# Kernel optimization log

Measured on AMD Instinct MI355X. Metric: run time of the kernel, lower is better.

## Reference

```python
import jax, jax.numpy as jnp
import numpy as np

N = 50000   # nodes
E = 800000  # edges (avg degree 16)
F_IN = 128
H = 128
L = 4
LN_EPS = 1e-5


def setup_inputs() -> dict:
    key = jax.random.key(0)
    ks = jax.random.split(key, 4)
    x = jax.random.normal(ks[0], (N, F_IN), dtype=jnp.float32)
    edge_index = jax.random.randint(ks[1], (2, E), 0, N)
    conv_w = jax.random.normal(ks[2], (L, F_IN, H), dtype=jnp.float32) * 0.05
    conv_b = jnp.zeros((L, H), dtype=jnp.float32)
    ln_g = jnp.ones((L, H), dtype=jnp.float32)
    ln_b = jnp.zeros((L, H), dtype=jnp.float32)
    head_w = jax.random.normal(ks[3], (H, 1), dtype=jnp.float32) * 0.05
    head_b = jnp.zeros((1,), dtype=jnp.float32)
    return {"x": x, "edge_index": edge_index, "conv_w": conv_w, "conv_b": conv_b,
            "ln_g": ln_g, "ln_b": ln_b, "head_w": head_w, "head_b": head_b}


def _layer_norm(h, g, b):
    mu = jnp.mean(h, axis=-1, keepdims=True)
    var = jnp.mean(jnp.square(h - mu), axis=-1, keepdims=True)
    return (h - mu) * jax.lax.rsqrt(var + LN_EPS) * g + b


def _gcn_conv(h, W, b, src, dst, inv_sqrt_deg, inv_deg):
    # PyG GCNConv: self-loops + symmetric normalization D^-1/2 (A+I) D^-1/2, then bias.
    hw = h @ W  # (N, H)
    norm = inv_sqrt_deg[src] * inv_sqrt_deg[dst]  # (E,)
    msg = hw[src] * norm[:, None]  # gather + edgewise scale
    agg = jax.ops.segment_sum(msg, dst, num_segments=N)  # scatter-add
    agg = agg + hw * inv_deg[:, None]  # self-loop term (norm = 1/deg)
    return agg + b


def reference(x, edge_index, conv_w, conv_b, ln_g, ln_b, head_w, head_b):
    src, dst = edge_index[0], edge_index[1]
    # degree on target nodes, including self-loop
    deg = jax.ops.segment_sum(jnp.ones((E,), x.dtype), dst, num_segments=N) + 1.0
    inv_sqrt_deg = jax.lax.rsqrt(deg)
    inv_deg = 1.0 / deg
    h = x
    for i in range(L):
        h = _gcn_conv(h, conv_w[i], conv_b[i], src, dst, inv_sqrt_deg, inv_deg)
        h = _layer_norm(h, ln_g[i], ln_b[i])
        if i != L - 1:
            h = jax.nn.gelu(h, approximate=False)
            # dropout is identity in eval mode
    scores = (h @ head_w + head_b).squeeze(-1)  # (N,)
    return scores, h
```

## Files before the change

### kernel.cpp

```cpp
#include <hip/hip_runtime.h>
#include <math.h>

#define N_NODES 50000
#define N_EDGES 800000
#define HDIM 128
#define NLAYERS 4
#define LN_EPS 1e-5f
#define EQUARTER (N_EDGES / 4)
#define SEG 64
#define FILLB ((EQUARTER + 255) / 256)
#define GEMMB ((N_NODES + 63) / 64)

typedef __attribute__((ext_vector_type(8))) short short8;
typedef __attribute__((ext_vector_type(4))) float floatx4;

__device__ __forceinline__ ushort f2bf(float x) {
    unsigned b = __float_as_uint(x);
    unsigned r = b + 0x7fffu + ((b >> 16) & 1u);
    return (ushort)(r >> 16);
}
__device__ __forceinline__ float2 bf2f2(unsigned u) {
    return make_float2(__uint_as_float(u << 16), __uint_as_float(u & 0xffff0000u));
}


__device__ __forceinline__ void fill_body(int bid, int tid, const int* __restrict__ src,
                                          const int* __restrict__ dst, int* __restrict__ cnt,
                                          ushort* __restrict__ csr16) {
    int t = bid * 256 + tid;
    if (t >= EQUARTER) return;
    int s0 = src[t],                d0 = dst[t];
    int s1 = src[t + EQUARTER],     d1 = dst[t + EQUARTER];
    int s2 = src[t + 2 * EQUARTER], d2 = dst[t + 2 * EQUARTER];
    int s3 = src[t + 3 * EQUARTER], d3 = dst[t + 3 * EQUARTER];
    int p0 = atomicAdd(&cnt[d0], 1);
    int p1 = atomicAdd(&cnt[d1], 1);
    int p2 = atomicAdd(&cnt[d2], 1);
    int p3 = atomicAdd(&cnt[d3], 1);
    if (p0 < SEG) csr16[d0 * SEG + p0] = (ushort)s0;
    if (p1 < SEG) csr16[d1 * SEG + p1] = (ushort)s1;
    if (p2 < SEG) csr16[d2 * SEG + p2] = (ushort)s2;
    if (p3 < SEG) csr16[d3 * SEG + p3] = (ushort)s3;
}

__global__ __launch_bounds__(256) void isd_kernel(const int* __restrict__ cnt,
                                                  float* __restrict__ isd,
                                                  float* __restrict__ ind) {
    int i = blockIdx.x * 256 + threadIdx.x;
    if (i < N_NODES) {
        float d = (float)cnt[i] + 1.0f;
        isd[i] = rsqrtf(d);
        ind[i] = 1.0f / d;
    }
}

__global__ __launch_bounds__(256) void bprep_kernel(const float* __restrict__ W,
                                                    ushort* __restrict__ bfrag) {
    int idx = blockIdx.x * 256 + threadIdx.x;
    if (idx >= NLAYERS * 4 * 8 * 64) return;
    int lane = idx & 63;
    int t = (idx >> 6) & 7;
    int s = (idx >> 9) & 3;
    int l = idx >> 11;
    int n = t * 16 + (lane & 15);
    int kb = s * 32 + (lane >> 4) * 8;
    const float* Wl = W + (size_t)l * HDIM * HDIM;
    union { uint4 q; ushort u[8]; } o;
#pragma unroll
    for (int j = 0; j < 8; ++j) o.u[j] = f2bf(Wl[(size_t)(kb + j) * HDIM + n]);
    *(uint4*)&bfrag[(size_t)idx * 8] = o.q;
}

template <bool A_FP32>
__device__ __forceinline__ void gemm_body(int bid, int tid, const void* __restrict__ Av,
                                          const ushort* __restrict__ bfrag,
                                          ushort* __restrict__ out) {
    int wave = tid >> 6, lane = tid & 63;
    int quad = lane >> 4, mrow = lane & 15;
    int rowBase = bid * 64 + wave * 16;
    int arow = rowBase + mrow;
    bool aok = arow < N_NODES;

    floatx4 acc[8];
#pragma unroll
    for (int t = 0; t < 8; ++t) acc[t] = (floatx4)0.f;

#pragma unroll
    for (int s = 0; s < 4; ++s) {
        union { short8 v; ushort u[8]; } af;
        if (A_FP32) {
            const float* A = (const float*)Av;
            if (aok) {
                const float* p = &A[(size_t)arow * HDIM + s * 32 + quad * 8];
#pragma unroll
                for (int j = 0; j < 8; ++j) af.u[j] = f2bf(p[j]);
            } else {
#pragma unroll
                for (int j = 0; j < 8; ++j) af.u[j] = 0;
            }
        } else {
            const ushort* A = (const ushort*)Av;
            if (aok) {
                af.v = *(const short8*)&A[(size_t)arow * HDIM + s * 32 + quad * 8];
            } else {
#pragma unroll
                for (int j = 0; j < 8; ++j) af.u[j] = 0;
            }
        }
#pragma unroll
        for (int t = 0; t < 8; ++t) {
            short8 bf = *(const short8*)&bfrag[(size_t)(((s * 8 + t) * 64) + lane) * 8];
            acc[t] = __builtin_amdgcn_mfma_f32_16x16x32_bf16(af.v, bf, acc[t], 0, 0, 0);
        }
    }
#pragma unroll
    for (int t = 0; t < 8; ++t) {
#pragma unroll
        for (int r = 0; r < 4; ++r) {
            int row = rowBase + quad * 4 + r;
            if (row < N_NODES) out[(size_t)row * HDIM + t * 16 + mrow] = f2bf(acc[t][r]);
        }
    }
}

__global__ __launch_bounds__(256) void fused0_kernel(
    const int* __restrict__ src, const int* __restrict__ dst, int* __restrict__ cnt,
    ushort* __restrict__ csr16, const float* __restrict__ x,
    const ushort* __restrict__ bfrag0, ushort* __restrict__ hw) {
    if (blockIdx.x < FILLB)
        fill_body(blockIdx.x, threadIdx.x, src, dst, cnt, csr16);
    else
        gemm_body<true>(blockIdx.x - FILLB, threadIdx.x, x, bfrag0, hw);
}

__global__ __launch_bounds__(256) void agg_ln_kernel(
    const uint2* __restrict__ hw2, const int* __restrict__ degcnt,
    const ushort* __restrict__ csr16, const float* __restrict__ isd,
    const float* __restrict__ ind, const float* __restrict__ conv_b,
    const float* __restrict__ ln_g, const float* __restrict__ ln_b,
    uint2* __restrict__ hout_bf, float* __restrict__ hout_f32,
    const float* __restrict__ head_w, const float* __restrict__ head_b,
    float* __restrict__ scores, int final_layer) {
    int wave = threadIdx.x >> 6;
    int lane = threadIdx.x & 63;
    int g = lane >> 5;
    int li = lane & 31;
    int n = blockIdx.x * 4 + wave;
    if (n >= N_NODES) return;
    int c = li * 4;

    float isd_n = isd[n], ind_n = ind[n];
    int rs = n * SEG;
    int deg = min(degcnt[n], SEG);

    float e0 = 0.f, e1 = 0.f, e2 = 0.f, e3 = 0.f;
    int sj = 0;
    float wj = 0.f;
    if (lane < deg) {
        sj = (int)csr16[rs + lane];
        wj = isd[sj];
    }
    for (int j = 0; j < deg; j += 8) {
#pragma unroll
        for (int t = 0; t < 4; ++t) {
            int idx = j + 2 * t + g;
            int s = __shfl(sj, idx);
            float w = __shfl(wj, idx);
            uint2 u = hw2[(size_t)s * 32 + li];
            float2 q0 = bf2f2(u.x), q1 = bf2f2(u.y);
            e0 = fmaf(q0.x, w, e0); e1 = fmaf(q0.y, w, e1);
            e2 = fmaf(q1.x, w, e2); e3 = fmaf(q1.y, w, e3);
        }
    }
    e0 += __shfl_xor(e0, 32); e1 += __shfl_xor(e1, 32);
    e2 += __shfl_xor(e2, 32); e3 += __shfl_xor(e3, 32);

    uint2 hv = hw2[(size_t)n * 32 + li];
    float2 h0 = bf2f2(hv.x), h1 = bf2f2(hv.y);
    float4 cb = *(const float4*)&conv_b[c];
    float a0 = fmaf(e0, isd_n, fmaf(h0.x, ind_n, cb.x));
    float a1 = fmaf(e1, isd_n, fmaf(h0.y, ind_n, cb.y));
    float a2 = fmaf(e2, isd_n, fmaf(h1.x, ind_n, cb.z));
    float a3 = fmaf(e3, isd_n, fmaf(h1.y, ind_n, cb.w));

    float sum = a0 + a1 + a2 + a3;
#pragma unroll
    for (int o = 1; o < 32; o <<= 1) sum += __shfl_xor(sum, o);
    float mu = sum * (1.0f / HDIM);
    float d0 = a0 - mu, d1 = a1 - mu, d2 = a2 - mu, d3 = a3 - mu;
    float vs = d0 * d0 + d1 * d1 + d2 * d2 + d3 * d3;
#pragma unroll
    for (int o = 1; o < 32; o <<= 1) vs += __shfl_xor(vs, o);
    float rstd = rsqrtf(vs * (1.0f / HDIM) + LN_EPS);
    float4 gv = *(const float4*)&ln_g[c];
    float4 bv = *(const float4*)&ln_b[c];
    float y0 = fmaf(d0 * rstd, gv.x, bv.x);
    float y1 = fmaf(d1 * rstd, gv.y, bv.y);
    float y2 = fmaf(d2 * rstd, gv.z, bv.z);
    float y3 = fmaf(d3 * rstd, gv.w, bv.w);

    if (!final_layer) {
#define GELU(v) ((v) = 0.5f * (v) * (1.0f + erff((v) * 0.70710678118654752f)))
        GELU(y0); GELU(y1); GELU(y2); GELU(y3);
#undef GELU
        if (g == 0) {
            uint2 ov;
            ov.x = (unsigned)f2bf(y0) | ((unsigned)f2bf(y1) << 16);
            ov.y = (unsigned)f2bf(y2) | ((unsigned)f2bf(y3) << 16);
            hout_bf[(size_t)n * 32 + li] = ov;
        }
    } else {
        if (g == 0)
            *(float4*)&hout_f32[(size_t)n * HDIM + c] = make_float4(y0, y1, y2, y3);
        float4 hwv = *(const float4*)&head_w[c];
        float p = y0 * hwv.x + y1 * hwv.y + y2 * hwv.z + y3 * hwv.w;
#pragma unroll
        for (int o = 1; o < 32; o <<= 1) p += __shfl_xor(p, o);
        if (lane == 0) scores[n] = p + head_b[0];
    }
}

__global__ __launch_bounds__(256) void layer_fused_kernel(
    const uint2* __restrict__ h2, const int* __restrict__ degcnt,
    const ushort* __restrict__ csr16, const float* __restrict__ isd,
    const float* __restrict__ ind, const ushort* __restrict__ bfrag,
    const float* __restrict__ conv_b, const float* __restrict__ ln_g,
    const float* __restrict__ ln_b, uint2* __restrict__ hout_bf,
    float* __restrict__ hout_f32, const float* __restrict__ head_w,
    const float* __restrict__ head_b, float* __restrict__ scores,
    int final_layer) {
    __shared__ float aggsf[64][132];
    int wave = threadIdx.x >> 6, lane = threadIdx.x & 63;
    int g = lane >> 5, li = lane & 31;

    for (int it = 0; it < 16; ++it) {
        int rblk = wave * 16 + it;
        int n = blockIdx.x * 64 + rblk;
        float a0 = 0.f, a1 = 0.f, a2 = 0.f, a3 = 0.f;
        if (n < N_NODES) {
            float isd_n = isd[n], ind_n = ind[n];
            int rs = n * SEG;
            int deg = min(degcnt[n], SEG);
            float e0 = 0.f, e1 = 0.f, e2 = 0.f, e3 = 0.f;
            int sj = 0;
            float wj = 0.f;
            if (lane < deg) {
                sj = (int)csr16[rs + lane];
                wj = isd[sj];
            }
            for (int j = 0; j < deg; j += 8) {
#pragma unroll
                for (int t = 0; t < 4; ++t) {
                    int idx = j + 2 * t + g;
                    int s = __shfl(sj, idx);
                    float w = __shfl(wj, idx);
                    uint2 u = h2[(size_t)s * 32 + li];
                    float2 q0 = bf2f2(u.x), q1 = bf2f2(u.y);
                    e0 = fmaf(q0.x, w, e0); e1 = fmaf(q0.y, w, e1);
                    e2 = fmaf(q1.x, w, e2); e3 = fmaf(q1.y, w, e3);
                }
            }
            e0 += __shfl_xor(e0, 32); e1 += __shfl_xor(e1, 32);
            e2 += __shfl_xor(e2, 32); e3 += __shfl_xor(e3, 32);
            uint2 hv = h2[(size_t)n * 32 + li];
            float2 h0 = bf2f2(hv.x), h1v = bf2f2(hv.y);
            a0 = fmaf(e0, isd_n, h0.x * ind_n);
            a1 = fmaf(e1, isd_n, h0.y * ind_n);
            a2 = fmaf(e2, isd_n, h1v.x * ind_n);
            a3 = fmaf(e3, isd_n, h1v.y * ind_n);
        }
        if (g == 0)
            *(float4*)&aggsf[rblk][li * 4] = make_float4(a0, a1, a2, a3);
    }

    int quad = lane >> 4, mrow = lane & 15;
    floatx4 acc[8];
#pragma unroll
    for (int t = 0; t < 8; ++t) acc[t] = (floatx4)0.f;
#pragma unroll
    for (int s = 0; s < 4; ++s) {
        const float* rowp = &aggsf[wave * 16 + mrow][s * 32 + quad * 8];
        float4 pa = *(const float4*)rowp;
        float4 pb = *(const float4*)(rowp + 4);
        float p[8] = {pa.x, pa.y, pa.z, pa.w, pb.x, pb.y, pb.z, pb.w};
        union { short8 v; ushort u[8]; } hi, lo;
#pragma unroll
        for (int j = 0; j < 8; ++j) {
            ushort h = f2bf(p[j]);
            hi.u[j] = h;
            float hf = __uint_as_float((unsigned)h << 16);
            lo.u[j] = f2bf(p[j] - hf);
        }
#pragma unroll
        for (int t = 0; t < 8; ++t) {
            short8 bf = *(const short8*)&bfrag[(size_t)(((s * 8 + t) * 64) + lane) * 8];
            acc[t] = __builtin_amdgcn_mfma_f32_16x16x32_bf16(lo.v, bf, acc[t], 0, 0, 0);
            acc[t] = __builtin_amdgcn_mfma_f32_16x16x32_bf16(hi.v, bf, acc[t], 0, 0, 0);
        }
    }

    {
        float cb[8];
#pragma unroll
        for (int t = 0; t < 8; ++t) cb[t] = conv_b[t * 16 + mrow];
#pragma unroll
        for (int t = 0; t < 8; ++t)
#pragma unroll
            for (int r = 0; r < 4; ++r)
                aggsf[wave * 16 + quad * 4 + r][t * 16 + mrow] = acc[t][r] + cb[t];
    }

    int c = li * 4;
    float4 gv = *(const float4*)&ln_g[c];
    float4 bv = *(const float4*)&ln_b[c];
    float4 hwv = *(const float4*)&head_w[c];
    for (int it = 0; it < 16; ++it) {
        int row = wave * 16 + it;
        int n = blockIdx.x * 64 + row;
        if (n >= N_NODES) continue;
        float4 v = *(const float4*)&aggsf[row][c];
        float a0 = v.x, a1 = v.y, a2 = v.z, a3 = v.w;

        float sum = a0 + a1 + a2 + a3;
#pragma unroll
        for (int o = 1; o < 32; o <<= 1) sum += __shfl_xor(sum, o);
        float mu = sum * (1.0f / HDIM);
        float d0 = a0 - mu, d1 = a1 - mu, d2 = a2 - mu, d3 = a3 - mu;
        float vs = d0 * d0 + d1 * d1 + d2 * d2 + d3 * d3;
#pragma unroll
        for (int o = 1; o < 32; o <<= 1) vs += __shfl_xor(vs, o);
        float rstd = rsqrtf(vs * (1.0f / HDIM) + LN_EPS);
        float y0 = fmaf(d0 * rstd, gv.x, bv.x);
        float y1 = fmaf(d1 * rstd, gv.y, bv.y);
        float y2 = fmaf(d2 * rstd, gv.z, bv.z);
        float y3 = fmaf(d3 * rstd, gv.w, bv.w);

        if (!final_layer) {
#define GELU(v) ((v) = 0.5f * (v) * (1.0f + erff((v) * 0.70710678118654752f)))
            GELU(y0); GELU(y1); GELU(y2); GELU(y3);
#undef GELU
            if (g == 0) {
                uint2 ov;
                ov.x = (unsigned)f2bf(y0) | ((unsigned)f2bf(y1) << 16);
                ov.y = (unsigned)f2bf(y2) | ((unsigned)f2bf(y3) << 16);
                hout_bf[(size_t)n * 32 + li] = ov;
            }
        } else {
            if (g == 0)
                *(float4*)&hout_f32[(size_t)n * HDIM + c] = make_float4(y0, y1, y2, y3);
            float p = y0 * hwv.x + y1 * hwv.y + y2 * hwv.z + y3 * hwv.w;
#pragma unroll
            for (int o = 1; o < 32; o <<= 1) p += __shfl_xor(p, o);
            if (lane == 0) scores[n] = p + head_b[0];
        }
    }
}


extern "C" void kernel_launch(void* const* d_in, const int* in_sizes, int n_in,
                              void* d_out, int out_size, void* d_ws, size_t ws_size,
                              hipStream_t stream) {
    const float* x      = (const float*)d_in[0];
    const int*   eidx   = (const int*)d_in[1];
    const float* conv_w = (const float*)d_in[2];
    const float* conv_b = (const float*)d_in[3];
    const float* ln_g   = (const float*)d_in[4];
    const float* ln_b   = (const float*)d_in[5];
    const float* head_w = (const float*)d_in[6];
    const float* head_b = (const float*)d_in[7];
    float* out = (float*)d_out;

    const int* src = eidx;
    const int* dst = eidx + N_EDGES;

    char* ws = (char*)d_ws;
    size_t o = 0;
    auto alloc = [&](size_t elems) {
        void* p = ws + o * 4;
        o += (elems + 15) & ~(size_t)15;
        return p;
    };
    int*      cnt      = (int*)alloc(N_NODES);
    float*    isd      = (float*)alloc(N_NODES);
    float*    ind      = (float*)alloc(N_NODES);
    ushort*   csr16    = (ushort*)alloc((size_t)N_NODES * SEG / 2);
    ushort*   bfrag    = (ushort*)alloc(NLAYERS * 4 * 8 * 64 * 8 / 2);
    unsigned* hw       = (unsigned*)alloc((size_t)N_NODES * 64);
    unsigned* hbuf     = (unsigned*)alloc((size_t)N_NODES * 64);

    hipMemsetAsync(cnt, 0, N_NODES * sizeof(int), stream);
    bprep_kernel<<<(NLAYERS * 4 * 8 * 64 + 255) / 256, 256, 0, stream>>>(conv_w, bfrag);
    fused0_kernel<<<FILLB + GEMMB, 256, 0, stream>>>(src, dst, cnt, csr16, x, bfrag,
                                                     (ushort*)hw);
    isd_kernel<<<(N_NODES + 255) / 256, 256, 0, stream>>>(cnt, isd, ind);

    agg_ln_kernel<<<(N_NODES + 3) / 4, 256, 0, stream>>>(
        (const uint2*)hw, cnt, csr16, isd, ind,
        conv_b, ln_g, ln_b,
        (uint2*)hbuf, out + N_NODES, head_w, head_b, out, 0);

    const unsigned* hin = hbuf;
    unsigned* hnext = hw;
    for (int l = 1; l < NLAYERS; ++l) {
        const ushort* bl = bfrag + (size_t)l * 4 * 8 * 64 * 8;
        int fin = (l == NLAYERS - 1) ? 1 : 0;
        layer_fused_kernel<<<GEMMB, 256, 0, stream>>>(
            (const uint2*)hin, cnt, csr16, isd, ind, bl,
            conv_b + (size_t)l * HDIM, ln_g + (size_t)l * HDIM, ln_b + (size_t)l * HDIM,
            (uint2*)hnext, out + N_NODES, head_w, head_b, out, fin);
        const unsigned* tmp = hin;
        hin = hnext;
        hnext = (unsigned*)tmp;
    }
}
```

Baseline: 389.5 us.

## Double the block to 512 threads and software-pipeline the neighbor gathers

Launches the fused layer kernel with 8 waves per block instead of 4. Each wave now aggregates 8 nodes instead of 16, and the MFMA tile work is split so each wave computes half of the output columns for a 16-row tile. The gather loop prefetches the next chunk of neighbor rows and the next node's CSR entries while the current chunk is accumulated, to hide global-load latency. It adds block-wide barriers between the phases and raises register pressure from the prefetch buffers.

```diff
diff --git a/kernel.cpp b/kernel.cpp
--- a/kernel.cpp
+++ b/kernel.cpp
@@ -220,7 +220,7 @@
     }
 }
 
-__global__ __launch_bounds__(256) void layer_fused_kernel(
+__global__ __launch_bounds__(512) void layer_fused_kernel(
     const uint2* __restrict__ h2, const int* __restrict__ degcnt,
     const ushort* __restrict__ csr16, const float* __restrict__ isd,
     const float* __restrict__ ind, const ushort* __restrict__ bfrag,
@@ -233,36 +233,58 @@
     int wave = threadIdx.x >> 6, lane = threadIdx.x & 63;
     int g = lane >> 5, li = lane & 31;
 
-    for (int it = 0; it < 16; ++it) {
-        int rblk = wave * 16 + it;
-        int n = blockIdx.x * 64 + rblk;
+    int nodeBase = blockIdx.x * 64 + wave * 8;
+    int deg_c = 0, sj_c = 0;
+    float wj_c = 0.f;
+    if (nodeBase < N_NODES) {
+        deg_c = min(degcnt[nodeBase], SEG);
+        int sraw = (int)csr16[nodeBase * SEG + lane];
+        sj_c = (lane < deg_c) ? sraw : 0;
+        float w = isd[sj_c];
+        wj_c = (lane < deg_c) ? w : 0.f;
+    }
+    for (int it = 0; it < 8; ++it) {
+        int n = nodeBase + it;
+        int deg = deg_c, sj = sj_c;
+        float wj = wj_c;
+        int deg_nx = 0, sraw_nx = 0;
+        if (it < 7 && (n + 1) < N_NODES) {
+            deg_nx = min(degcnt[n + 1], SEG);
+            sraw_nx = (int)csr16[(n + 1) * SEG + lane];
+        }
         float a0 = 0.f, a1 = 0.f, a2 = 0.f, a3 = 0.f;
         if (n < N_NODES) {
             float isd_n = isd[n], ind_n = ind[n];
-            int rs = n * SEG;
-            int deg = min(degcnt[n], SEG);
+            uint2 hv = h2[(size_t)n * 32 + li];
             float e0 = 0.f, e1 = 0.f, e2 = 0.f, e3 = 0.f;
-            int sj = 0;
-            float wj = 0.f;
-            if (lane < deg) {
-                sj = (int)csr16[rs + lane];
-                wj = isd[sj];
+            uint2 u[4];
+#pragma unroll
+            for (int t = 0; t < 4; ++t) {
+                int s = __shfl(sj, 2 * t + g);
+                u[t] = h2[(size_t)s * 32 + li];
             }
             for (int j = 0; j < deg; j += 8) {
+                uint2 un[4];
+                int jn = j + 8;
+                bool more = jn < deg;
+                if (more) {
+#pragma unroll
+                    for (int t = 0; t < 4; ++t) {
+                        int s = __shfl(sj, jn + 2 * t + g);
+                        un[t] = h2[(size_t)s * 32 + li];
+                    }
+                }
 #pragma unroll
                 for (int t = 0; t < 4; ++t) {
-                    int idx = j + 2 * t + g;
-                    int s = __shfl(sj, idx);
-                    float w = __shfl(wj, idx);
-                    uint2 u = h2[(size_t)s * 32 + li];
-                    float2 q0 = bf2f2(u.x), q1 = bf2f2(u.y);
+                    float w = __shfl(wj, j + 2 * t + g);
+                    float2 q0 = bf2f2(u[t].x), q1 = bf2f2(u[t].y);
                     e0 = fmaf(q0.x, w, e0); e1 = fmaf(q0.y, w, e1);
                     e2 = fmaf(q1.x, w, e2); e3 = fmaf(q1.y, w, e3);
                 }
+                if (more) { u[0] = un[0]; u[1] = un[1]; u[2] = un[2]; u[3] = un[3]; }
             }
             e0 += __shfl_xor(e0, 32); e1 += __shfl_xor(e1, 32);
             e2 += __shfl_xor(e2, 32); e3 += __shfl_xor(e3, 32);
-            uint2 hv = h2[(size_t)n * 32 + li];
             float2 h0 = bf2f2(hv.x), h1v = bf2f2(hv.y);
             a0 = fmaf(e0, isd_n, h0.x * ind_n);
             a1 = fmaf(e1, isd_n, h0.y * ind_n);
@@ -270,16 +292,23 @@
             a3 = fmaf(e3, isd_n, h1v.y * ind_n);
         }
         if (g == 0)
-            *(float4*)&aggsf[rblk][li * 4] = make_float4(a0, a1, a2, a3);
-    }
+            *(float4*)&aggsf[wave * 8 + it][li * 4] = make_float4(a0, a1, a2, a3);
+        deg_c = deg_nx;
+        sj_c = (lane < deg_nx) ? sraw_nx : 0;
+        float w = isd[sj_c];
+        wj_c = (lane < deg_nx) ? w : 0.f;
+    }
+    __syncthreads();
 
     int quad = lane >> 4, mrow = lane & 15;
-    floatx4 acc[8];
-#pragma unroll
-    for (int t = 0; t < 8; ++t) acc[t] = (floatx4)0.f;
+    int rtile = (wave >> 1) * 16;
+    int chalf = (wave & 1) * 4;
+    floatx4 acc[4];
+#pragma unroll
+    for (int t = 0; t < 4; ++t) acc[t] = (floatx4)0.f;
 #pragma unroll
     for (int s = 0; s < 4; ++s) {
-        const float* rowp = &aggsf[wave * 16 + mrow][s * 32 + quad * 8];
+        const float* rowp = &aggsf[rtile + mrow][s * 32 + quad * 8];
         float4 pa = *(const float4*)rowp;
         float4 pb = *(const float4*)(rowp + 4);
         float p[8] = {pa.x, pa.y, pa.z, pa.w, pb.x, pb.y, pb.z, pb.w};
@@ -292,30 +321,33 @@
             lo.u[j] = f2bf(p[j] - hf);
         }
 #pragma unroll
-        for (int t = 0; t < 8; ++t) {
+        for (int t4 = 0; t4 < 4; ++t4) {
+            int t = chalf + t4;
             short8 bf = *(const short8*)&bfrag[(size_t)(((s * 8 + t) * 64) + lane) * 8];
-            acc[t] = __builtin_amdgcn_mfma_f32_16x16x32_bf16(lo.v, bf, acc[t], 0, 0, 0);
-            acc[t] = __builtin_amdgcn_mfma_f32_16x16x32_bf16(hi.v, bf, acc[t], 0, 0, 0);
-        }
-    }
+            acc[t4] = __builtin_amdgcn_mfma_f32_16x16x32_bf16(lo.v, bf, acc[t4], 0, 0, 0);
+            acc[t4] = __builtin_amdgcn_mfma_f32_16x16x32_bf16(hi.v, bf, acc[t4], 0, 0, 0);
+        }
+    }
+    __syncthreads();
 
     {
-        float cb[8];
-#pragma unroll
-        for (int t = 0; t < 8; ++t) cb[t] = conv_b[t * 16 + mrow];
-#pragma unroll
-        for (int t = 0; t < 8; ++t)
+        float cb[4];
+#pragma unroll
+        for (int t4 = 0; t4 < 4; ++t4) cb[t4] = conv_b[(chalf + t4) * 16 + mrow];
+#pragma unroll
+        for (int t4 = 0; t4 < 4; ++t4)
 #pragma unroll
             for (int r = 0; r < 4; ++r)
-                aggsf[wave * 16 + quad * 4 + r][t * 16 + mrow] = acc[t][r] + cb[t];
-    }
+                aggsf[rtile + quad * 4 + r][(chalf + t4) * 16 + mrow] = acc[t4][r] + cb[t4];
+    }
+    __syncthreads();
 
     int c = li * 4;
     float4 gv = *(const float4*)&ln_g[c];
     float4 bv = *(const float4*)&ln_b[c];
     float4 hwv = *(const float4*)&head_w[c];
-    for (int it = 0; it < 16; ++it) {
-        int row = wave * 16 + it;
+    for (int it = 0; it < 8; ++it) {
+        int row = wave * 8 + it;
         int n = blockIdx.x * 64 + row;
         if (n >= N_NODES) continue;
         float4 v = *(const float4*)&aggsf[row][c];
@@ -404,7 +436,7 @@
     for (int l = 1; l < NLAYERS; ++l) {
         const ushort* bl = bfrag + (size_t)l * 4 * 8 * 64 * 8;
         int fin = (l == NLAYERS - 1) ? 1 : 0;
-        layer_fused_kernel<<<GEMMB, 256, 0, stream>>>(
+        layer_fused_kernel<<<GEMMB, 512, 0, stream>>>(
             (const uint2*)hin, cnt, csr16, isd, ind, bl,
             conv_b + (size_t)l * HDIM, ln_g + (size_t)l * HDIM, ln_b + (size_t)l * HDIM,
             (uint2*)hnext, out + N_NODES, head_w, head_b, out, fin);
```

New measurement: 401.1 us. +3.0%, slower.
